# Kernel tuning notes

Measured on AMD Instinct MI355X. Metric: run time of the kernel, lower is better.

The kernel has to match this reference:

```python
import jax, jax.numpy as jnp
import numpy as np

N = 50000      # nodes
E = 800000     # edges (before self loops)
F_IN = 128
HID = 32
HEADS = 4
OUT_DIM = 1
NEG_SLOPE = 0.2


def gat_conv(x, edge_src, edge_dst, W, a_src, a_dst, bias):
    """PyG GATConv (concat=True, self-loops already appended to edge lists).
    x: [N, Fin], W: [Fin, H*D], a_src/a_dst: [H, D], bias: [H*D]."""
    H, D = a_src.shape
    h = (x @ W).reshape(N, H, D)                      # [N, H, D]
    alpha_src = jnp.einsum('nhd,hd->nh', h, a_src)    # [N, H]
    alpha_dst = jnp.einsum('nhd,hd->nh', h, a_dst)    # [N, H]
    e = alpha_src[edge_src] + alpha_dst[edge_dst]     # [Et, H]
    e = jnp.where(e > 0, e, NEG_SLOPE * e)            # leaky_relu(0.2)
    # softmax over edges grouped by destination node
    m = jax.ops.segment_max(e, edge_dst, num_segments=N)  # [N, H]
    e = jnp.exp(e - jax.lax.stop_gradient(m)[edge_dst])
    s = jax.ops.segment_sum(e, edge_dst, num_segments=N)  # [N, H]
    alpha = e / (s[edge_dst] + 1e-16)                 # [Et, H]
    msg = h[edge_src] * alpha[:, :, None]             # [Et, H, D]
    out = jax.ops.segment_sum(msg, edge_dst, num_segments=N)  # [N, H, D]
    return out.reshape(N, H * D) + bias


def setup_inputs() -> dict:
    key = jax.random.key(0)
    ks = jax.random.split(key, 16)
    HD = HEADS * HID
    def glorot(k, shape, fan_in):
        return jax.random.normal(k, shape, dtype=jnp.float32) / np.sqrt(fan_in)
    inp = {
        'x': jax.random.normal(ks[0], (N, F_IN), dtype=jnp.float32),
        'edge_index': jax.random.randint(ks[1], (2, E), 0, N, dtype=jnp.int64 if jax.config.jax_enable_x64 else jnp.int32),
        'W1': glorot(ks[2], (F_IN, HD), F_IN),
        'a_src1': glorot(ks[3], (HEADS, HID), HID),
        'a_dst1': glorot(ks[4], (HEADS, HID), HID),
        'b1': jnp.zeros((HD,), dtype=jnp.float32),
        'W2': glorot(ks[5], (HD, HD), HD),
        'a_src2': glorot(ks[6], (HEADS, HID), HID),
        'a_dst2': glorot(ks[7], (HEADS, HID), HID),
        'b2': jnp.zeros((HD,), dtype=jnp.float32),
        'Wc1': glorot(ks[8], (HD, HID), HD),
        'bc1': jnp.zeros((HID,), dtype=jnp.float32),
        'Wc2': glorot(ks[9], (HID, OUT_DIM), HID),
        'bc2': jnp.zeros((OUT_DIM,), dtype=jnp.float32),
    }
    return inp


def reference(x, edge_index, W1, a_src1, a_dst1, b1, W2, a_src2, a_dst2, b2,
              Wc1, bc1, Wc2, bc2):
    # PyG add_self_loops=True: append (i -> i) for every node
    loops = jnp.arange(N, dtype=edge_index.dtype)
    src = jnp.concatenate([edge_index[0], loops])
    dst = jnp.concatenate([edge_index[1], loops])
    h = gat_conv(x, src, dst, W1, a_src1, a_dst1, b1)
    h = jax.nn.relu(h)
    h = gat_conv(h, src, dst, W2, a_src2, a_dst2, b2)
    h = jax.nn.relu(h)
    # classifier (dropout is identity at eval)
    h = h @ Wc1 + bc1
    h = h @ Wc2 + bc2
    return jax.nn.sigmoid(h)
```

## Files before the change

kernel.cpp:

```cpp
#include <hip/hip_runtime.h>
#include <hip/hip_bf16.h>
#include <math.h>

#define NEG_SLOPE 0.2f

__device__ __forceinline__ unsigned short f2bf(float f) {
    unsigned int u = __float_as_uint(f);
    u = (u + 0x7fffu + ((u >> 16) & 1u)) >> 16;
    return (unsigned short)u;
}
__device__ __forceinline__ float bflo(unsigned int p) {
    return __uint_as_float(p << 16);
}
__device__ __forceinline__ float bfhi(unsigned int p) {
    return __uint_as_float(p & 0xffff0000u);
}

__device__ __forceinline__ void gemm_alpha_body(
    float* __restrict__ xt,
    const float* __restrict__ X, const float* __restrict__ W,
    const float* __restrict__ a_src, const float* __restrict__ a_dst,
    unsigned short* __restrict__ Hb, float* __restrict__ as_out,
    float* __restrict__ ad_out, int N, int n0, int t)
{
    {
        const float4* src = (const float4*)(X + (size_t)n0 * 128);
        float4* dst = (float4*)xt;
        int rows = N - n0; if (rows > 32) rows = 32;
        int maxv = rows * 32;
        #pragma unroll
        for (int i = 0; i < 4; ++i) {
            int idx = t + i * 256;
            int g = idx < maxv ? idx : maxv - 1;
            dst[idx] = src[g];
        }
    }
    __syncthreads();

    int rg = t >> 5;
    int c  = t & 31;
    int j0 = c * 4;

    float a00=0.f,a01=0.f,a02=0.f,a03=0.f;
    float a10=0.f,a11=0.f,a12=0.f,a13=0.f;
    float a20=0.f,a21=0.f,a22=0.f,a23=0.f;
    float a30=0.f,a31=0.f,a32=0.f,a33=0.f;

    #pragma unroll 4
    for (int k = 0; k < 128; ++k) {
        float4 w = *(const float4*)(W + k * 128 + j0);
        float x0 = xt[(rg     ) * 128 + k];
        float x1 = xt[(rg +  8) * 128 + k];
        float x2 = xt[(rg + 16) * 128 + k];
        float x3 = xt[(rg + 24) * 128 + k];
        a00 = fmaf(x0, w.x, a00); a01 = fmaf(x0, w.y, a01);
        a02 = fmaf(x0, w.z, a02); a03 = fmaf(x0, w.w, a03);
        a10 = fmaf(x1, w.x, a10); a11 = fmaf(x1, w.y, a11);
        a12 = fmaf(x1, w.z, a12); a13 = fmaf(x1, w.w, a13);
        a20 = fmaf(x2, w.x, a20); a21 = fmaf(x2, w.y, a21);
        a22 = fmaf(x2, w.z, a22); a23 = fmaf(x2, w.w, a23);
        a30 = fmaf(x3, w.x, a30); a31 = fmaf(x3, w.y, a31);
        a32 = fmaf(x3, w.z, a32); a33 = fmaf(x3, w.w, a33);
    }

    float4 asv = *(const float4*)(a_src + j0);
    float4 adv = *(const float4*)(a_dst + j0);
    int head = c >> 3;
    int wlane = (c & 7) == 0;

    #pragma unroll
    for (int rr = 0; rr < 4; ++rr) {
        float b0, b1, b2, b3;
        if (rr == 0) { b0=a00; b1=a01; b2=a02; b3=a03; }
        else if (rr == 1) { b0=a10; b1=a11; b2=a12; b3=a13; }
        else if (rr == 2) { b0=a20; b1=a21; b2=a22; b3=a23; }
        else { b0=a30; b1=a31; b2=a32; b3=a33; }
        int row = n0 + rg + rr * 8;
        bool valid = row < N;
        if (valid) {
            unsigned int lo = (unsigned int)f2bf(b0) | ((unsigned int)f2bf(b1) << 16);
            unsigned int hi = (unsigned int)f2bf(b2) | ((unsigned int)f2bf(b3) << 16);
            *(uint2*)(Hb + (size_t)row * 128 + j0) = make_uint2(lo, hi);
        }
        float ps = b0*asv.x + b1*asv.y + b2*asv.z + b3*asv.w;
        float pd = b0*adv.x + b1*adv.y + b2*adv.z + b3*adv.w;
        ps += __shfl_xor(ps, 1, 64); pd += __shfl_xor(pd, 1, 64);
        ps += __shfl_xor(ps, 2, 64); pd += __shfl_xor(pd, 2, 64);
        ps += __shfl_xor(ps, 4, 64); pd += __shfl_xor(pd, 4, 64);
        if (wlane && valid) {
            as_out[row * 4 + head] = ps;
            ad_out[row * 4 + head] = pd;
        }
    }
}

__global__ __launch_bounds__(256) void gemm_alpha_kernel(
    const float* __restrict__ X, const float* __restrict__ W,
    const float* __restrict__ a_src, const float* __restrict__ a_dst,
    unsigned short* __restrict__ Hb, float* __restrict__ as_out,
    float* __restrict__ ad_out, int N)
{
    __shared__ float xt[32 * 128];
    gemm_alpha_body(xt, X, W, a_src, a_dst, Hb, as_out, ad_out, N,
                    blockIdx.x * 32, threadIdx.x);
}

__global__ __launch_bounds__(256) void gemm_fill_kernel(
    const float* __restrict__ X, const float* __restrict__ W,
    const float* __restrict__ a_src, const float* __restrict__ a_dst,
    unsigned short* __restrict__ Hb, float* __restrict__ as_out,
    float* __restrict__ ad_out, int N,
    const int* __restrict__ esrc, const int* __restrict__ edst, int E, int Et,
    const int* __restrict__ offs, const int* __restrict__ rank,
    int* __restrict__ csr, int gemmBlocks, int NS)
{
    __shared__ float xt[32 * 128];
    int g  = blockIdx.x >> 3;
    int l8 = blockIdx.x & 7;
    if ((g & 1) == 0) {
        int gb = (g >> 1) * 8 + l8;
        if (gb < gemmBlocks)
            gemm_alpha_body(xt, X, W, a_src, a_dst, Hb, as_out, ad_out, N,
                            gb * 32, threadIdx.x);
    } else {
        int slice = g >> 1;
        if (slice >= NS) return;
        int rlo = (int)(((long long)N * l8) >> 3);
        int rhi = (int)(((long long)N * (l8 + 1)) >> 3);
        int e0 = (int)((long long)Et * slice / NS);
        int e1 = (int)((long long)Et * (slice + 1) / NS);
        for (int e = e0 + threadIdx.x; e < e1; e += 256) {
            int d = (e < E) ? edst[e] : (e - E);
            if (d >= rlo && d < rhi) {
                int s = (e < E) ? esrc[e] : d;
                csr[offs[d] + rank[e]] = s;
            }
        }
    }
}

__global__ __launch_bounds__(256) void zero_int_kernel(int* __restrict__ p, int n)
{
    int i = blockIdx.x * 256 + threadIdx.x;
    if (i < n) p[i] = 0;
}

__global__ __launch_bounds__(256) void count_rank_kernel(
    const int* __restrict__ edst, int E, int Et,
    int* __restrict__ cnt, int* __restrict__ rank)
{
    int e = blockIdx.x * 256 + threadIdx.x;
    if (e >= Et) return;
    int d = (e < E) ? edst[e] : (e - E);
    rank[e] = atomicAdd(&cnt[d], 1);
}

__global__ __launch_bounds__(256) void scan_block_kernel(
    const int* __restrict__ in, int* __restrict__ out,
    int* __restrict__ bsum, int n)
{
    __shared__ int sh[256];
    int i = blockIdx.x * 256 + threadIdx.x;
    int v = (i < n) ? in[i] : 0;
    sh[threadIdx.x] = v;
    __syncthreads();
    #pragma unroll
    for (int off = 1; off < 256; off <<= 1) {
        int t = 0;
        if (threadIdx.x >= off) t = sh[threadIdx.x - off];
        __syncthreads();
        if (threadIdx.x >= off) sh[threadIdx.x] += t;
        __syncthreads();
    }
    if (i < n) out[i] = sh[threadIdx.x] - v;
    if (threadIdx.x == 255) bsum[blockIdx.x] = sh[255];
}

__global__ __launch_bounds__(256) void scan_add_kernel(
    int* __restrict__ offs, const int* __restrict__ bsum, int n)
{
    int i = blockIdx.x * 256 + threadIdx.x;
    if (i < n) offs[i] += bsum[blockIdx.x];
}

__global__ __launch_bounds__(256) void gat_fused_kernel(
    const unsigned short* __restrict__ Hb, const int* __restrict__ csr,
    const int* __restrict__ offs, const int* __restrict__ cnt,
    const float* __restrict__ as, const float* __restrict__ ad,
    const float* __restrict__ bias, float* __restrict__ out, int N)
{
    __shared__ float wtab[4 * 64 * 4];
    __shared__ int   stab[4 * 64];

    int wv = threadIdx.x >> 6;
    int d = blockIdx.x * 4 + wv;
    if (d >= N) return;
    int lane = threadIdx.x & 63;
    int start = offs[d];
    int deg = cnt[d];
    float4 adv = *(const float4*)(ad + d * 4);
    int h = lane >> 4;
    int f0 = lane * 2;

    float m0 = -INFINITY, m1 = -INFINITY, m2 = -INFINITY, m3 = -INFINITY;
    float s0 = 0.f, s1 = 0.f, s2 = 0.f, s3 = 0.f;
    float acc0 = 0.f, acc1 = 0.f;

    const float* wbase = wtab + (wv * 64) * 4 + h;
    const int*   sbase = stab + wv * 64;

    for (int c0 = 0; c0 < deg; c0 += 64) {
        int rem = deg - c0;
        int len = rem < 64 ? rem : 64;
        bool valid = lane < len;
        int sidx = valid ? csr[start + c0 + lane] : 0;
        float4 av = *(const float4*)(as + sidx * 4);
        float e0 = av.x + adv.x; e0 = e0 > 0.f ? e0 : NEG_SLOPE * e0;
        float e1 = av.y + adv.y; e1 = e1 > 0.f ? e1 : NEG_SLOPE * e1;
        float e2 = av.z + adv.z; e2 = e2 > 0.f ? e2 : NEG_SLOPE * e2;
        float e3 = av.w + adv.w; e3 = e3 > 0.f ? e3 : NEG_SLOPE * e3;
        if (!valid) { e0 = e1 = e2 = e3 = -INFINITY; }

        float c0m = e0, c1m = e1, c2m = e2, c3m = e3;
        #pragma unroll
        for (int off = 32; off; off >>= 1) {
            c0m = fmaxf(c0m, __shfl_xor(c0m, off, 64));
            c1m = fmaxf(c1m, __shfl_xor(c1m, off, 64));
            c2m = fmaxf(c2m, __shfl_xor(c2m, off, 64));
            c3m = fmaxf(c3m, __shfl_xor(c3m, off, 64));
        }
        float nm0 = fmaxf(m0, c0m), nm1 = fmaxf(m1, c1m);
        float nm2 = fmaxf(m2, c2m), nm3 = fmaxf(m3, c3m);
        float r0 = __expf(m0 - nm0), r1 = __expf(m1 - nm1);
        float r2 = __expf(m2 - nm2), r3 = __expf(m3 - nm3);
        m0 = nm0; m1 = nm1; m2 = nm2; m3 = nm3;

        float w0 = valid ? __expf(e0 - m0) : 0.f;
        float w1 = valid ? __expf(e1 - m1) : 0.f;
        float w2 = valid ? __expf(e2 - m2) : 0.f;
        float w3 = valid ? __expf(e3 - m3) : 0.f;

        float t0 = w0, t1 = w1, t2 = w2, t3 = w3;
        #pragma unroll
        for (int off = 32; off; off >>= 1) {
            t0 += __shfl_xor(t0, off, 64);
            t1 += __shfl_xor(t1, off, 64);
            t2 += __shfl_xor(t2, off, 64);
            t3 += __shfl_xor(t3, off, 64);
        }
        s0 = s0 * r0 + t0; s1 = s1 * r1 + t1;
        s2 = s2 * r2 + t2; s3 = s3 * r3 + t3;
        float rs = h == 0 ? r0 : (h == 1 ? r1 : (h == 2 ? r2 : r3));
        acc0 *= rs;
        acc1 *= rs;

        ((float4*)wtab)[threadIdx.x] = make_float4(w0, w1, w2, w3);
        stab[threadIdx.x] = sidx;

        int kk = 0;
        for (; kk + 4 <= len; kk += 4) {
            int sk0 = sbase[kk+0], sk1 = sbase[kk+1];
            int sk2 = sbase[kk+2], sk3 = sbase[kk+3];
            float wa = wbase[(kk+0)*4], wb = wbase[(kk+1)*4];
            float wc = wbase[(kk+2)*4], wd = wbase[(kk+3)*4];
            unsigned int p0 = *(const unsigned int*)(Hb + (size_t)sk0 * 128 + f0);
            unsigned int p1 = *(const unsigned int*)(Hb + (size_t)sk1 * 128 + f0);
            unsigned int p2 = *(const unsigned int*)(Hb + (size_t)sk2 * 128 + f0);
            unsigned int p3 = *(const unsigned int*)(Hb + (size_t)sk3 * 128 + f0);
            acc0 = fmaf(wa, bflo(p0), acc0); acc1 = fmaf(wa, bfhi(p0), acc1);
            acc0 = fmaf(wb, bflo(p1), acc0); acc1 = fmaf(wb, bfhi(p1), acc1);
            acc0 = fmaf(wc, bflo(p2), acc0); acc1 = fmaf(wc, bfhi(p2), acc1);
            acc0 = fmaf(wd, bflo(p3), acc0); acc1 = fmaf(wd, bfhi(p3), acc1);
        }
        for (; kk < len; ++kk) {
            int sk = sbase[kk];
            float wk = wbase[kk*4];
            unsigned int p = *(const unsigned int*)(Hb + (size_t)sk * 128 + f0);
            acc0 = fmaf(wk, bflo(p), acc0);
            acc1 = fmaf(wk, bfhi(p), acc1);
        }
    }

    float sh = h == 0 ? s0 : (h == 1 ? s1 : (h == 2 ? s2 : s3));
    float inv = 1.f / (sh + 1e-16f);
    float2 bv = *(const float2*)(bias + f0);
    float o0 = acc0 * inv + bv.x;
    float o1 = acc1 * inv + bv.y;
    *(float2*)(out + (size_t)d * 128 + f0) = make_float2(fmaxf(o0, 0.f), fmaxf(o1, 0.f));
}

__global__ __launch_bounds__(256) void classifier_kernel(
    const float* __restrict__ X, const float* __restrict__ Wc1,
    const float* __restrict__ bc1, const float* __restrict__ Wc2,
    const float* __restrict__ bc2, float* __restrict__ out, int N)
{
    int n = blockIdx.x * 8 + (threadIdx.x >> 5);
    if (n >= N) return;
    int j = threadIdx.x & 31;
    const float* xrow = X + (size_t)n * 128;
    float acc = bc1[j];
    #pragma unroll 8
    for (int k = 0; k < 128; ++k)
        acc = fmaf(xrow[k], Wc1[k * 32 + j], acc);
    float y = acc * Wc2[j];
    #pragma unroll
    for (int off = 16; off; off >>= 1) y += __shfl_xor(y, off, 64);
    if (j == 0)
        out[n] = 1.0f / (1.0f + expf(-(y + bc2[0])));
}

extern "C" void kernel_launch(void* const* d_in, const int* in_sizes, int n_in,
                              void* d_out, int out_size, void* d_ws, size_t ws_size,
                              hipStream_t stream)
{
    const float* x      = (const float*)d_in[0];
    const int*   eidx   = (const int*)d_in[1];
    const float* W1     = (const float*)d_in[2];
    const float* a_src1 = (const float*)d_in[3];
    const float* a_dst1 = (const float*)d_in[4];
    const float* b1     = (const float*)d_in[5];
    const float* W2     = (const float*)d_in[6];
    const float* a_src2 = (const float*)d_in[7];
    const float* a_dst2 = (const float*)d_in[8];
    const float* b2     = (const float*)d_in[9];
    const float* Wc1    = (const float*)d_in[10];
    const float* bc1    = (const float*)d_in[11];
    const float* Wc2    = (const float*)d_in[12];
    const float* bc2    = (const float*)d_in[13];

    int N  = in_sizes[0] / 128;
    int E  = in_sizes[1] / 2;
    int Et = E + N;
    const int* esrc = eidx;
    const int* edst = eidx + E;

    char* wsb = (char*)d_ws;
    unsigned short* Hb = (unsigned short*)wsb;  wsb += (size_t)N * 128 * 2;
    float*  f1_buf = (float*)wsb;   wsb += (size_t)N * 128 * 4;
    float*  as_buf = (float*)wsb;   wsb += (size_t)N * 4 * 4;
    float*  ad_buf = (float*)wsb;   wsb += (size_t)N * 4 * 4;
    int*    cnt    = (int*)wsb;     wsb += (size_t)N * 4;
    int*    offs   = (int*)wsb;     wsb += (size_t)N * 4;
    int*    bsum   = (int*)wsb;     wsb += 512 * 4;
    int*    csr    = (int*)wsb;     wsb += (size_t)Et * 4;
    int*    rank   = (int*)wsb;     wsb += (size_t)Et * 4;

    int nbN = (N + 255) / 256;
    int nbE = (Et + 255) / 256;
    int gemmBlocks = (N + 31) / 32;
    int gemmGroups = (gemmBlocks + 7) / 8;
    int NS = gemmGroups;
    int fusedGrid = gemmGroups * 2 * 8;

    zero_int_kernel<<<nbN, 256, 0, stream>>>(cnt, N);
    count_rank_kernel<<<nbE, 256, 0, stream>>>(edst, E, Et, cnt, rank);
    scan_block_kernel<<<nbN, 256, 0, stream>>>(cnt, offs, bsum, N);
    scan_block_kernel<<<1, 256, 0, stream>>>(bsum, bsum, &bsum[300], nbN);
    scan_add_kernel<<<nbN, 256, 0, stream>>>(offs, bsum, N);

    gemm_fill_kernel<<<fusedGrid, 256, 0, stream>>>(
        x, W1, a_src1, a_dst1, Hb, as_buf, ad_buf, N,
        esrc, edst, E, Et, offs, rank, csr, gemmBlocks, NS);
    gat_fused_kernel<<<(N + 3) / 4, 256, 0, stream>>>(Hb, csr, offs, cnt,
                                                      as_buf, ad_buf, b1, f1_buf, N);
    gemm_alpha_kernel<<<gemmBlocks, 256, 0, stream>>>(f1_buf, W2, a_src2, a_dst2,
                                                      Hb, as_buf, ad_buf, N);
    gat_fused_kernel<<<(N + 3) / 4, 256, 0, stream>>>(Hb, csr, offs, cnt,
                                                      as_buf, ad_buf, b2, f1_buf, N);

    classifier_kernel<<<(N + 7) / 8, 256, 0, stream>>>(f1_buf, Wc1, bc1, Wc2, bc2,
                                                       (float*)d_out, N);
}
```

Before: 366.7 us.

## Map 16 lanes per destination node in GAT aggregation and precompute CSR positions

```diff
diff --git a/kernel.cpp b/kernel.cpp
--- a/kernel.cpp
+++ b/kernel.cpp
@@ -110,8 +110,8 @@
     const float* __restrict__ a_src, const float* __restrict__ a_dst,
     unsigned short* __restrict__ Hb, float* __restrict__ as_out,
     float* __restrict__ ad_out, int N,
-    const int* __restrict__ esrc, const int* __restrict__ edst, int E, int Et,
-    const int* __restrict__ offs, const int* __restrict__ rank,
+    const int* __restrict__ esrc, int E, int Et,
+    const int* __restrict__ offs, const int* __restrict__ pos,
     int* __restrict__ csr, int gemmBlocks, int NS)
 {
     __shared__ float xt[32 * 128];
@@ -127,13 +127,15 @@
         if (slice >= NS) return;
         int rlo = (int)(((long long)N * l8) >> 3);
         int rhi = (int)(((long long)N * (l8 + 1)) >> 3);
+        int csrLo = offs[rlo];
+        int csrHi = (rhi < N) ? offs[rhi] : Et;
         int e0 = (int)((long long)Et * slice / NS);
         int e1 = (int)((long long)Et * (slice + 1) / NS);
         for (int e = e0 + threadIdx.x; e < e1; e += 256) {
-            int d = (e < E) ? edst[e] : (e - E);
-            if (d >= rlo && d < rhi) {
-                int s = (e < E) ? esrc[e] : d;
-                csr[offs[d] + rank[e]] = s;
+            int p = pos[e];
+            if (p >= csrLo && p < csrHi) {
+                int s = (e < E) ? esrc[e] : (e - E);
+                csr[p] = s;
             }
         }
     }
@@ -153,6 +155,16 @@
     if (e >= Et) return;
     int d = (e < E) ? edst[e] : (e - E);
     rank[e] = atomicAdd(&cnt[d], 1);
+}
+
+__global__ __launch_bounds__(256) void pos_kernel(
+    const int* __restrict__ edst, int E, int Et,
+    const int* __restrict__ offs, int* __restrict__ rank)
+{
+    int e = blockIdx.x * 256 + threadIdx.x;
+    if (e >= Et) return;
+    int d = (e < E) ? edst[e] : (e - E);
+    rank[e] = offs[d] + rank[e];
 }
 
 __global__ __launch_bounds__(256) void scan_block_kernel(
@@ -189,31 +201,33 @@
     const float* __restrict__ as, const float* __restrict__ ad,
     const float* __restrict__ bias, float* __restrict__ out, int N)
 {
-    __shared__ float wtab[4 * 64 * 4];
+    __shared__ float wtab[4 * 256];
     __shared__ int   stab[4 * 64];
 
-    int wv = threadIdx.x >> 6;
-    int d = blockIdx.x * 4 + wv;
+    int t = threadIdx.x;
+    int wv = t >> 6;
+    int g  = (t >> 4) & 3;
+    int q  = t & 15;
+    int d = blockIdx.x * 16 + (t >> 4);
     if (d >= N) return;
-    int lane = threadIdx.x & 63;
     int start = offs[d];
     int deg = cnt[d];
     float4 adv = *(const float4*)(ad + d * 4);
-    int h = lane >> 4;
-    int f0 = lane * 2;
+    int h = q >> 2;
+    int f0 = q * 8;
 
     float m0 = -INFINITY, m1 = -INFINITY, m2 = -INFINITY, m3 = -INFINITY;
     float s0 = 0.f, s1 = 0.f, s2 = 0.f, s3 = 0.f;
-    float acc0 = 0.f, acc1 = 0.f;
-
-    const float* wbase = wtab + (wv * 64) * 4 + h;
-    const int*   sbase = stab + wv * 64;
-
-    for (int c0 = 0; c0 < deg; c0 += 64) {
+    float acc0=0.f,acc1=0.f,acc2=0.f,acc3=0.f,acc4=0.f,acc5=0.f,acc6=0.f,acc7=0.f;
+
+    const float* wbase = wtab + wv * 256 + g * 4 + h;
+    const int*   sbase = stab + wv * 64 + g * 16;
+
+    for (int c0 = 0; c0 < deg; c0 += 16) {
         int rem = deg - c0;
-        int len = rem < 64 ? rem : 64;
-        bool valid = lane < len;
-        int sidx = valid ? csr[start + c0 + lane] : 0;
+        int len = rem < 16 ? rem : 16;
+        bool valid = q < len;
+        int sidx = valid ? csr[start + c0 + q] : 0;
         float4 av = *(const float4*)(as + sidx * 4);
         float e0 = av.x + adv.x; e0 = e0 > 0.f ? e0 : NEG_SLOPE * e0;
         float e1 = av.y + adv.y; e1 = e1 > 0.f ? e1 : NEG_SLOPE * e1;
@@ -223,7 +237,7 @@
 
         float c0m = e0, c1m = e1, c2m = e2, c3m = e3;
         #pragma unroll
-        for (int off = 32; off; off >>= 1) {
+        for (int off = 8; off; off >>= 1) {
             c0m = fmaxf(c0m, __shfl_xor(c0m, off, 64));
             c1m = fmaxf(c1m, __shfl_xor(c1m, off, 64));
             c2m = fmaxf(c2m, __shfl_xor(c2m, off, 64));
@@ -242,7 +256,7 @@
 
         float t0 = w0, t1 = w1, t2 = w2, t3 = w3;
         #pragma unroll
-        for (int off = 32; off; off >>= 1) {
+        for (int off = 8; off; off >>= 1) {
             t0 += __shfl_xor(t0, off, 64);
             t1 += __shfl_xor(t1, off, 64);
             t2 += __shfl_xor(t2, off, 64);
@@ -251,42 +265,64 @@
         s0 = s0 * r0 + t0; s1 = s1 * r1 + t1;
         s2 = s2 * r2 + t2; s3 = s3 * r3 + t3;
         float rs = h == 0 ? r0 : (h == 1 ? r1 : (h == 2 ? r2 : r3));
-        acc0 *= rs;
-        acc1 *= rs;
-
-        ((float4*)wtab)[threadIdx.x] = make_float4(w0, w1, w2, w3);
-        stab[threadIdx.x] = sidx;
+        acc0 *= rs; acc1 *= rs; acc2 *= rs; acc3 *= rs;
+        acc4 *= rs; acc5 *= rs; acc6 *= rs; acc7 *= rs;
+
+        ((float4*)wtab)[wv * 64 + q * 4 + g] = make_float4(w0, w1, w2, w3);
+        stab[wv * 64 + g * 16 + q] = sidx;
 
         int kk = 0;
         for (; kk + 4 <= len; kk += 4) {
             int sk0 = sbase[kk+0], sk1 = sbase[kk+1];
             int sk2 = sbase[kk+2], sk3 = sbase[kk+3];
-            float wa = wbase[(kk+0)*4], wb = wbase[(kk+1)*4];
-            float wc = wbase[(kk+2)*4], wd = wbase[(kk+3)*4];
-            unsigned int p0 = *(const unsigned int*)(Hb + (size_t)sk0 * 128 + f0);
-            unsigned int p1 = *(const unsigned int*)(Hb + (size_t)sk1 * 128 + f0);
-            unsigned int p2 = *(const unsigned int*)(Hb + (size_t)sk2 * 128 + f0);
-            unsigned int p3 = *(const unsigned int*)(Hb + (size_t)sk3 * 128 + f0);
-            acc0 = fmaf(wa, bflo(p0), acc0); acc1 = fmaf(wa, bfhi(p0), acc1);
-            acc0 = fmaf(wb, bflo(p1), acc0); acc1 = fmaf(wb, bfhi(p1), acc1);
-            acc0 = fmaf(wc, bflo(p2), acc0); acc1 = fmaf(wc, bfhi(p2), acc1);
-            acc0 = fmaf(wd, bflo(p3), acc0); acc1 = fmaf(wd, bfhi(p3), acc1);
+            float wa = wbase[(kk+0)*16], wb = wbase[(kk+1)*16];
+            float wc = wbase[(kk+2)*16], wd = wbase[(kk+3)*16];
+            uint4 p0 = *(const uint4*)(Hb + (size_t)sk0 * 128 + f0);
+            uint4 p1 = *(const uint4*)(Hb + (size_t)sk1 * 128 + f0);
+            uint4 p2 = *(const uint4*)(Hb + (size_t)sk2 * 128 + f0);
+            uint4 p3 = *(const uint4*)(Hb + (size_t)sk3 * 128 + f0);
+            acc0 = fmaf(wa, bflo(p0.x), acc0); acc1 = fmaf(wa, bfhi(p0.x), acc1);
+            acc2 = fmaf(wa, bflo(p0.y), acc2); acc3 = fmaf(wa, bfhi(p0.y), acc3);
+            acc4 = fmaf(wa, bflo(p0.z), acc4); acc5 = fmaf(wa, bfhi(p0.z), acc5);
+            acc6 = fmaf(wa, bflo(p0.w), acc6); acc7 = fmaf(wa, bfhi(p0.w), acc7);
+            acc0 = fmaf(wb, bflo(p1.x), acc0); acc1 = fmaf(wb, bfhi(p1.x), acc1);
+            acc2 = fmaf(wb, bflo(p1.y), acc2); acc3 = fmaf(wb, bfhi(p1.y), acc3);
+            acc4 = fmaf(wb, bflo(p1.z), acc4); acc5 = fmaf(wb, bfhi(p1.z), acc5);
+            acc6 = fmaf(wb, bflo(p1.w), acc6); acc7 = fmaf(wb, bfhi(p1.w), acc7);
+            acc0 = fmaf(wc, bflo(p2.x), acc0); acc1 = fmaf(wc, bfhi(p2.x), acc1);
+            acc2 = fmaf(wc, bflo(p2.y), acc2); acc3 = fmaf(wc, bfhi(p2.y), acc3);
+            acc4 = fmaf(wc, bflo(p2.z), acc4); acc5 = fmaf(wc, bfhi(p2.z), acc5);
+            acc6 = fmaf(wc, bflo(p2.w), acc6); acc7 = fmaf(wc, bfhi(p2.w), acc7);
+            acc0 = fmaf(wd, bflo(p3.x), acc0); acc1 = fmaf(wd, bfhi(p3.x), acc1);
+            acc2 = fmaf(wd, bflo(p3.y), acc2); acc3 = fmaf(wd, bfhi(p3.y), acc3);
+            acc4 = fmaf(wd, bflo(p3.z), acc4); acc5 = fmaf(wd, bfhi(p3.z), acc5);
+            acc6 = fmaf(wd, bflo(p3.w), acc6); acc7 = fmaf(wd, bfhi(p3.w), acc7);
         }
         for (; kk < len; ++kk) {
             int sk = sbase[kk];
-            float wk = wbase[kk*4];
-            unsigned int p = *(const unsigned int*)(Hb + (size_t)sk * 128 + f0);
-            acc0 = fmaf(wk, bflo(p), acc0);
-            acc1 = fmaf(wk, bfhi(p), acc1);
+            float wk = wbase[kk*16];
+            uint4 p = *(const uint4*)(Hb + (size_t)sk * 128 + f0);
+            acc0 = fmaf(wk, bflo(p.x), acc0); acc1 = fmaf(wk, bfhi(p.x), acc1);
+            acc2 = fmaf(wk, bflo(p.y), acc2); acc3 = fmaf(wk, bfhi(p.y), acc3);
+            acc4 = fmaf(wk, bflo(p.z), acc4); acc5 = fmaf(wk, bfhi(p.z), acc5);
+            acc6 = fmaf(wk, bflo(p.w), acc6); acc7 = fmaf(wk, bfhi(p.w), acc7);
         }
     }
 
     float sh = h == 0 ? s0 : (h == 1 ? s1 : (h == 2 ? s2 : s3));
     float inv = 1.f / (sh + 1e-16f);
-    float2 bv = *(const float2*)(bias + f0);
-    float o0 = acc0 * inv + bv.x;
-    float o1 = acc1 * inv + bv.y;
-    *(float2*)(out + (size_t)d * 128 + f0) = make_float2(fmaxf(o0, 0.f), fmaxf(o1, 0.f));
+    float4 bA = *(const float4*)(bias + f0);
+    float4 bB = *(const float4*)(bias + f0 + 4);
+    float4 oA = make_float4(fmaxf(acc0 * inv + bA.x, 0.f),
+                            fmaxf(acc1 * inv + bA.y, 0.f),
+                            fmaxf(acc2 * inv + bA.z, 0.f),
+                            fmaxf(acc3 * inv + bA.w, 0.f));
+    float4 oB = make_float4(fmaxf(acc4 * inv + bB.x, 0.f),
+                            fmaxf(acc5 * inv + bB.y, 0.f),
+                            fmaxf(acc6 * inv + bB.z, 0.f),
+                            fmaxf(acc7 * inv + bB.w, 0.f));
+    *(float4*)(out + (size_t)d * 128 + f0)     = oA;
+    *(float4*)(out + (size_t)d * 128 + f0 + 4) = oB;
 }
 
 __global__ __launch_bounds__(256) void classifier_kernel(
@@ -357,16 +393,17 @@
     scan_block_kernel<<<nbN, 256, 0, stream>>>(cnt, offs, bsum, N);
     scan_block_kernel<<<1, 256, 0, stream>>>(bsum, bsum, &bsum[300], nbN);
     scan_add_kernel<<<nbN, 256, 0, stream>>>(offs, bsum, N);
+    pos_kernel<<<nbE, 256, 0, stream>>>(edst, E, Et, offs, rank);
 
     gemm_fill_kernel<<<fusedGrid, 256, 0, stream>>>(
         x, W1, a_src1, a_dst1, Hb, as_buf, ad_buf, N,
-        esrc, edst, E, Et, offs, rank, csr, gemmBlocks, NS);
-    gat_fused_kernel<<<(N + 3) / 4, 256, 0, stream>>>(Hb, csr, offs, cnt,
-                                                      as_buf, ad_buf, b1, f1_buf, N);
+        esrc, E, Et, offs, rank, csr, gemmBlocks, NS);
+    gat_fused_kernel<<<(N + 15) / 16, 256, 0, stream>>>(Hb, csr, offs, cnt,
+                                                        as_buf, ad_buf, b1, f1_buf, N);
     gemm_alpha_kernel<<<gemmBlocks, 256, 0, stream>>>(f1_buf, W2, a_src2, a_dst2,
                                                       Hb, as_buf, ad_buf, N);
-    gat_fused_kernel<<<(N + 3) / 4, 256, 0, stream>>>(Hb, csr, offs, cnt,
-                                                      as_buf, ad_buf, b2, f1_buf, N);
+    gat_fused_kernel<<<(N + 15) / 16, 256, 0, stream>>>(Hb, csr, offs, cnt,
+                                                        as_buf, ad_buf, b2, f1_buf, N);
 
     classifier_kernel<<<(N + 7) / 8, 256, 0, stream>>>(f1_buf, Wc1, bc1, Wc2, bc2,
                                                        (float*)d_out, N);
```

New measurement: 368.5 us. About the same (+0.5%).
